# Performance work log

Measured on AMD Instinct MI355X. Metric: run time of the kernel, lower is better.

## Reference

```python
import jax, jax.numpy as jnp
import numpy as np

IN_DIM = 128
OUT_DIM = 128
ATTN_DIM = 64
N_REL = 200
N_NODE = 50000
N_EDGE = 500000
N_QUERY = 64
COE_TIMEDIFF = 0.2  # computed in torch code but unused downstream


def setup_inputs() -> dict:
    key = jax.random.key(0)
    ks = jax.random.split(key, 24)
    # edges: [E,7] with columns (r_idx, _, rel, _, tau, sub, obj)
    r_idx = jax.random.randint(ks[0], (N_EDGE,), 0, N_QUERY)
    rel = jax.random.randint(ks[1], (N_EDGE,), 0, 2 * N_REL + 1)
    tau = jax.random.randint(ks[2], (N_EDGE,), -1, 366)  # -1 triggers the where() fallback
    sub = jax.random.randint(ks[3], (N_EDGE,), 0, N_NODE)
    obj = jax.random.randint(ks[4], (N_EDGE,), 0, N_NODE)
    fill = jnp.zeros((N_EDGE,), jnp.int64 if jax.config.jax_enable_x64 else jnp.int32)
    edges = jnp.stack([r_idx, fill, rel, fill, tau, sub, obj], axis=1)
    s = 1.0 / np.sqrt(IN_DIM)
    sa = 1.0 / np.sqrt(ATTN_DIM)
    return {
        "q_sub": jax.random.randint(ks[5], (N_QUERY,), 0, N_NODE),
        "q_rel": jax.random.randint(ks[6], (N_QUERY,), 0, 2 * N_REL + 1),
        "q_tau": jax.random.randint(ks[7], (N_QUERY,), 0, 366),
        "hidden": jax.random.normal(ks[8], (N_NODE, IN_DIM), jnp.float32),
        "edges": edges,
        "n_node": N_NODE,
        "old_nodes_new_idx": jax.random.randint(ks[9], (10000,), 0, N_NODE),
        "rela_embed": jax.random.normal(ks[10], (2 * N_REL + 1, IN_DIM), jnp.float32),
        "Ws": jax.random.normal(ks[11], (IN_DIM, ATTN_DIM), jnp.float32) * s,
        "Wr": jax.random.normal(ks[12], (IN_DIM, ATTN_DIM), jnp.float32) * s,
        "Wqr_W": jax.random.normal(ks[13], (IN_DIM, ATTN_DIM), jnp.float32) * s,
        "Wqr_b": jax.random.normal(ks[14], (ATTN_DIM,), jnp.float32) * s,
        "Wtau": jax.random.normal(ks[15], (IN_DIM, ATTN_DIM), jnp.float32) * s,
        "w_alpha_W": jax.random.normal(ks[16], (ATTN_DIM, 1), jnp.float32) * sa,
        "w_alpha_b": jax.random.normal(ks[17], (1,), jnp.float32) * sa,
        "Wh": jax.random.normal(ks[18], (IN_DIM, OUT_DIM), jnp.float32) * s,
        "wt1": jax.random.normal(ks[19], (1, IN_DIM), jnp.float32),
        "bt1": jax.random.normal(ks[20], (1, IN_DIM), jnp.float32),
        "wt2": jax.random.normal(ks[21], (1, IN_DIM), jnp.float32),
        "bt2": jax.random.normal(ks[22], (1, IN_DIM), jnp.float32),
    }


def reference(q_sub, q_rel, q_tau, hidden, edges, n_node, old_nodes_new_idx,
              rela_embed, Ws, Wr, Wqr_W, Wqr_b, Wtau, w_alpha_W, w_alpha_b,
              Wh, wt1, bt1, wt2, bt2):
    r_idx = edges[:, 0]
    rel = edges[:, 2]
    tau = edges[:, 4]
    sub = edges[:, 5]
    obj = edges[:, 6]
    hs = hidden[sub]                      # [E, in_dim] gather
    hr = rela_embed[rel]                  # [E, in_dim]
    h_qr = rela_embed[q_rel][r_idx]       # [E, in_dim]
    taus_q = q_tau[r_idx]
    tau = jnp.where(tau >= 0, tau, taus_q)
    delta_tau = (tau - taus_q).astype(hidden.dtype)[:, None]  # [E,1]
    h_tau = wt1 * delta_tau + bt1 + jnp.sin(wt2 * delta_tau + bt2)  # [E, in_dim]
    message = hs + hr + h_tau
    pre = jax.nn.relu(hs @ Ws + hr @ Wr + (h_qr @ Wqr_W + Wqr_b) + h_tau @ Wtau)
    alpha = jax.nn.sigmoid(pre @ w_alpha_W + w_alpha_b)  # [E,1]
    msg_agg = jax.ops.segment_sum(alpha * message, obj, num_segments=n_node)
    return msg_agg @ Wh  # act is identity by default
```

## Files before the change

kernel.cpp:

```cpp
#include <hip/hip_runtime.h>
#include <hip/hip_fp16.h>

#define IN_DIM   128
#define OUT_DIM  128
#define ATTN_DIM 64
#define N_RELV   401
#define N_NODE   50000
#define N_EDGE   500000
#define N_QUERY  64
#define N_DT     731
#define CAP      40

#define NBW_NODE 782
#define NBW_REL  7
#define NBW_DT   12
#define NBW_QR   1
#define NBW_ZERO 13
#define RB0      NBW_NODE
#define DB0      (NBW_NODE + NBW_REL)
#define QB0      (DB0 + NBW_DT)
#define ZB0      (QB0 + NBW_QR)
#define FB0      (ZB0 + NBW_ZERO)
#define NB_TOT   (FB0 + 1)

typedef unsigned short ushort_t;
typedef unsigned int   uint_t;
typedef __attribute__((ext_vector_type(8))) short v8s;
typedef __attribute__((ext_vector_type(4))) float v4f;

__device__ __forceinline__ int clampi(int v, int lo, int hi) {
    return v < lo ? lo : (v > hi ? hi : v);
}
__device__ __forceinline__ float bu2f(ushort_t u) {
    union { uint_t i; float f; } v; v.i = ((uint_t)u) << 16; return v.f;
}
__device__ __forceinline__ float blo(uint_t u) { return bu2f((ushort_t)(u & 0xffff)); }
__device__ __forceinline__ float bhi(uint_t u) { return bu2f((ushort_t)(u >> 16)); }
__device__ __forceinline__ ushort_t f2bu(float f) {
    union { float f; uint_t i; } v; v.f = f;
    const uint_t x = v.i;
    return (ushort_t)((x + 0x7fffu + ((x >> 16) & 1u)) >> 16);
}
__device__ __forceinline__ uint_t cvtpk(float a, float b) {
    uint_t r;
    asm("v_cvt_pk_bf16_f32 %0, %1, %2" : "=v"(r) : "v"(a), "v"(b));
    return r;
}

__device__ __forceinline__ int swz_byte(int row, int byte_in_row) {
    return (row * 256 + byte_in_row) ^ ((row & 7) << 4);
}

__device__ __forceinline__ void stage_w64(ushort_t* shw, const float* __restrict__ W,
                                          int tid) {
    #pragma unroll
    for (int i = 0; i < 4; ++i) {
        const int pi = tid + 256 * i;
        const int kp = pi >> 4;
        const int n4 = (pi & 15) * 4;
        const float4 A = *(const float4*)(W + (size_t)(2 * kp) * 64 + n4);
        const float4 B = *(const float4*)(W + (size_t)(2 * kp + 1) * 64 + n4);
        const float Aa[4] = {A.x, A.y, A.z, A.w};
        const float Ba[4] = {B.x, B.y, B.z, B.w};
        #pragma unroll
        for (int j = 0; j < 4; ++j)
            *(uint_t*)((char*)shw + swz_byte(n4 + j, kp * 4)) = cvtpk(Aa[j], Ba[j]);
    }
}
__device__ __forceinline__ void stage_w128(ushort_t* shw, const float* __restrict__ W,
                                           int tid) {
    #pragma unroll
    for (int i = 0; i < 8; ++i) {
        const int pi = tid + 256 * i;
        const int kp = pi >> 5;
        const int n4 = (pi & 31) * 4;
        const float4 A = *(const float4*)(W + (size_t)(2 * kp) * 128 + n4);
        const float4 B = *(const float4*)(W + (size_t)(2 * kp + 1) * 128 + n4);
        const float Aa[4] = {A.x, A.y, A.z, A.w};
        const float Ba[4] = {B.x, B.y, B.z, B.w};
        #pragma unroll
        for (int j = 0; j < 4; ++j)
            *(uint_t*)((char*)shw + swz_byte(64 + n4 + j, kp * 4)) = cvtpk(Aa[j], Ba[j]);
    }
}
__device__ __forceinline__ void load_x_rows(const float* __restrict__ X, int rowc,
                                            int q, v8s hfr[4]) {
    #pragma unroll
    for (int c = 0; c < 4; ++c) {
        const float4 f0 = *(const float4*)(X + (size_t)rowc * 128 + 32 * c + 8 * q);
        const float4 f1 = *(const float4*)(X + (size_t)rowc * 128 + 32 * c + 8 * q + 4);
        union { v8s s; uint4 u; } uu;
        uu.u = make_uint4(cvtpk(f0.x, f0.y), cvtpk(f0.z, f0.w),
                          cvtpk(f1.x, f1.y), cvtpk(f1.z, f1.w));
        hfr[c] = uu.s;
    }
}
__device__ __forceinline__ void mfma_store(const ushort_t* shw, const v8s hfr[4],
                                           int row, int Nlim,
                                           ushort_t* __restrict__ attn_out,
                                           ushort_t* __restrict__ msg_out,
                                           int m16, int q) {
    #pragma unroll
    for (int t = 0; t < 12; ++t) {
        v4f acc = {0.f, 0.f, 0.f, 0.f};
        #pragma unroll
        for (int c = 0; c < 4; ++c) {
            const v8s wfr = *(const v8s*)((const char*)shw +
                              swz_byte(16 * t + m16, (32 * c + 8 * q) * 2));
            acc = __builtin_amdgcn_mfma_f32_16x16x32_bf16(wfr, hfr[c], acc, 0, 0, 0);
        }
        if (row < Nlim) {
            const uint_t u0 = cvtpk(acc[0], acc[1]);
            const uint_t u1 = cvtpk(acc[2], acc[3]);
            const int dim = 16 * t + 4 * q;
            if (dim < 64)
                *(uint2*)(attn_out + (size_t)row * 64 + dim) = make_uint2(u0, u1);
            else
                *(uint2*)(msg_out + (size_t)row * 128 + (dim - 64)) = make_uint2(u0, u1);
        }
    }
}

__global__ __launch_bounds__(256) void fused_pre(
    const float* __restrict__ hidden, const float* __restrict__ Ws,
    const float* __restrict__ Wh,   const float* __restrict__ rela,
    const float* __restrict__ Wr,   const float* __restrict__ Wtau,
    const float* __restrict__ wt1,  const float* __restrict__ bt1,
    const float* __restrict__ wt2,  const float* __restrict__ bt2,
    const int* __restrict__ q_rel,  const float* __restrict__ WqrW,
    const float* __restrict__ Wqrb, const int* __restrict__ edges,
    ushort_t* __restrict__ node_attn, ushort_t* __restrict__ node_msg,
    ushort_t* __restrict__ rel_attn,  ushort_t* __restrict__ rel_msg,
    ushort_t* __restrict__ dt_attn,   ushort_t* __restrict__ dt_msg,
    ushort_t* __restrict__ Xqr,
    int* __restrict__ flag, int* __restrict__ cnt, int* __restrict__ ovfn)
{
    __shared__ ushort_t shw[192 * 128];
    const int bid = blockIdx.x, tid = threadIdx.x;
    const int wid = tid >> 6, lane = tid & 63;
    const int m16 = lane & 15, q = lane >> 4;

    if (bid < NBW_NODE) {
        stage_w64 (shw, Ws, tid);
        stage_w128(shw, Wh, tid);
        __syncthreads();
        const int row  = bid * 64 + wid * 16 + m16;
        const int rowc = row < N_NODE ? row : N_NODE - 1;
        v8s hfr[4];
        load_x_rows(hidden, rowc, q, hfr);
        mfma_store(shw, hfr, row, N_NODE, node_attn, node_msg, m16, q);
    } else if (bid < DB0) {
        stage_w64 (shw, Wr, tid);
        stage_w128(shw, Wh, tid);
        __syncthreads();
        const int row  = (bid - RB0) * 64 + wid * 16 + m16;
        const int rowc = row < N_RELV ? row : N_RELV - 1;
        v8s hfr[4];
        load_x_rows(rela, rowc, q, hfr);
        mfma_store(shw, hfr, row, N_RELV, rel_attn, rel_msg, m16, q);
    } else if (bid < QB0) {
        stage_w64 (shw, Wtau, tid);
        stage_w128(shw, Wh, tid);
        __syncthreads();
        const int row  = (bid - DB0) * 64 + wid * 16 + m16;
        const int rowc = row < N_DT ? row : N_DT - 1;
        const float dtv = (float)(rowc - 365);
        v8s hfr[4];
        #pragma unroll
        for (int c = 0; c < 4; ++c) {
            const int o = 32 * c + 8 * q;
            const float4 w1a = *(const float4*)(wt1 + o), w1b = *(const float4*)(wt1 + o + 4);
            const float4 b1a = *(const float4*)(bt1 + o), b1b = *(const float4*)(bt1 + o + 4);
            const float4 w2a = *(const float4*)(wt2 + o), w2b = *(const float4*)(wt2 + o + 4);
            const float4 b2a = *(const float4*)(bt2 + o), b2b = *(const float4*)(bt2 + o + 4);
            const float h0 = w1a.x * dtv + b1a.x + sinf(w2a.x * dtv + b2a.x);
            const float h1 = w1a.y * dtv + b1a.y + sinf(w2a.y * dtv + b2a.y);
            const float h2 = w1a.z * dtv + b1a.z + sinf(w2a.z * dtv + b2a.z);
            const float h3 = w1a.w * dtv + b1a.w + sinf(w2a.w * dtv + b2a.w);
            const float h4 = w1b.x * dtv + b1b.x + sinf(w2b.x * dtv + b2b.x);
            const float h5 = w1b.y * dtv + b1b.y + sinf(w2b.y * dtv + b2b.y);
            const float h6 = w1b.z * dtv + b1b.z + sinf(w2b.z * dtv + b2b.z);
            const float h7 = w1b.w * dtv + b1b.w + sinf(w2b.w * dtv + b2b.w);
            union { v8s s; uint4 u; } uu;
            uu.u = make_uint4(cvtpk(h0, h1), cvtpk(h2, h3), cvtpk(h4, h5), cvtpk(h6, h7));
            hfr[c] = uu.s;
        }
        mfma_store(shw, hfr, row, N_DT, dt_attn, dt_msg, m16, q);
    } else if (bid < ZB0) {
        int* ok = (int*)shw;
        if (tid == 0) *ok = 1;
        __syncthreads();
        int badv = 0;
        for (int t = tid; t < 1000; t += 256) {
            const int w = edges[2 * t + 1];
            if (w != 0 && w != -1) badv = 1;
        }
        if (badv) *ok = 0;
        __syncthreads();
        const int i64 = *ok;
        __syncthreads();

        stage_w64(shw, WqrW, tid);
        __syncthreads();
        const int qrow = wid * 16 + m16;
        const int relq = clampi(q_rel[i64 ? 2 * qrow : qrow], 0, N_RELV - 1);
        v8s hfr[4];
        load_x_rows(rela, relq, q, hfr);
        #pragma unroll
        for (int t = 0; t < 4; ++t) {
            v4f acc = {0.f, 0.f, 0.f, 0.f};
            #pragma unroll
            for (int c = 0; c < 4; ++c) {
                const v8s wfr = *(const v8s*)((const char*)shw +
                                  swz_byte(16 * t + m16, (32 * c + 8 * q) * 2));
                acc = __builtin_amdgcn_mfma_f32_16x16x32_bf16(wfr, hfr[c], acc, 0, 0, 0);
            }
            const int dim = 16 * t + 4 * q;
            const float4 bi = *(const float4*)(Wqrb + dim);
            const uint_t u0 = cvtpk(acc[0] + bi.x, acc[1] + bi.y);
            const uint_t u1 = cvtpk(acc[2] + bi.z, acc[3] + bi.w);
            *(uint2*)(Xqr + (size_t)qrow * 64 + dim) = make_uint2(u0, u1);
        }
    } else if (bid < FB0) {
        int4* c4 = (int4*)cnt;
        const int b = (bid - ZB0) * 256 + tid;
        #pragma unroll
        for (int k = 0; k < 4; ++k) {
            const int i4 = b * 4 + k;
            if (i4 < N_NODE / 4) c4[i4] = make_int4(0, 0, 0, 0);
        }
    } else {
        int* ok = (int*)shw;
        if (tid == 0) *ok = 0;
        __syncthreads();
        int badv = 0;
        for (int t = tid; t < 1000; t += 256) {
            const int w = edges[2 * t + 1];
            if (w != 0 && w != -1) badv = 1;
        }
        if (badv) *ok = 1;
        __syncthreads();
        if (tid == 0) { flag[0] = (*ok == 0) ? 1 : 0; ovfn[0] = 0; }
    }
}

__device__ __forceinline__ float dot8(uint4 xs, uint4 xr, uint4 xt, uint4 xq,
                                      float4 wA, float4 wB)
{
    float s0, s1, v;
    s0 = blo(xs.x) + blo(xr.x) + blo(xt.x) + blo(xq.x);
    s1 = bhi(xs.x) + bhi(xr.x) + bhi(xt.x) + bhi(xq.x);
    v  = fmaxf(s0, 0.f) * wA.x + fmaxf(s1, 0.f) * wA.y;
    s0 = blo(xs.y) + blo(xr.y) + blo(xt.y) + blo(xq.y);
    s1 = bhi(xs.y) + bhi(xr.y) + bhi(xt.y) + bhi(xq.y);
    v += fmaxf(s0, 0.f) * wA.z + fmaxf(s1, 0.f) * wA.w;
    s0 = blo(xs.z) + blo(xr.z) + blo(xt.z) + blo(xq.z);
    s1 = bhi(xs.z) + bhi(xr.z) + bhi(xt.z) + bhi(xq.z);
    v += fmaxf(s0, 0.f) * wB.x + fmaxf(s1, 0.f) * wB.y;
    s0 = blo(xs.w) + blo(xr.w) + blo(xt.w) + blo(xq.w);
    s1 = bhi(xs.w) + bhi(xr.w) + bhi(xt.w) + bhi(xq.w);
    v += fmaxf(s0, 0.f) * wB.z + fmaxf(s1, 0.f) * wB.w;
    return v;
}

__global__ __launch_bounds__(256) void alpha_scatter(
    const int* __restrict__ edges, const int* __restrict__ q_tau,
    const ushort_t* __restrict__ node_attn, const ushort_t* __restrict__ rel_attn,
    const ushort_t* __restrict__ dt_attn,  const ushort_t* __restrict__ Xqr,
    const float* __restrict__ w_alpha_W, const float* __restrict__ w_alpha_b,
    const int* __restrict__ flag, int* __restrict__ cnt,
    int2* __restrict__ meta, int* __restrict__ ovfn, int4* __restrict__ ovfl)
{
    const int g   = threadIdx.x & 7;
    const int grp = threadIdx.x >> 3;
    const int e0r = blockIdx.x * 128 + grp * 4;
    const int e0  = e0r <= N_EDGE - 4 ? e0r : N_EDGE - 4;
    const int i64 = flag[0];

    const float4 wA = *(const float4*)(w_alpha_W + 8 * g);
    const float4 wB = *(const float4*)(w_alpha_W + 8 * g + 4);

    int r0, rel0, tau0, sub0, obj0, r1, rel1, tau1, sub1, obj1;
    int r2, rel2, tau2, sub2, obj2, r3, rel3, tau3, sub3, obj3;
    if (!i64) {
        const int4 ev = *(const int4*)(edges + (size_t)e0 * 7 + 4 * (g < 6 ? g : 6));
        #define GETF(j) __shfl(((j) & 3) == 0 ? ev.x : ((j) & 3) == 1 ? ev.y : \
                               ((j) & 3) == 2 ? ev.z : ev.w, (j) >> 2, 8)
        r0 = GETF(0);  rel0 = GETF(2);  tau0 = GETF(4);  sub0 = GETF(5);  obj0 = GETF(6);
        r1 = GETF(7);  rel1 = GETF(9);  tau1 = GETF(11); sub1 = GETF(12); obj1 = GETF(13);
        r2 = GETF(14); rel2 = GETF(16); tau2 = GETF(18); sub2 = GETF(19); obj2 = GETF(20);
        r3 = GETF(21); rel3 = GETF(23); tau3 = GETF(25); sub3 = GETF(26); obj3 = GETF(27);
        #undef GETF
    } else {
        const int* E0 = edges + (size_t)(e0    ) * 14;
        const int* E1 = edges + (size_t)(e0 + 1) * 14;
        const int* E2 = edges + (size_t)(e0 + 2) * 14;
        const int* E3 = edges + (size_t)(e0 + 3) * 14;
        r0 = E0[0]; rel0 = E0[4]; tau0 = E0[8]; sub0 = E0[10]; obj0 = E0[12];
        r1 = E1[0]; rel1 = E1[4]; tau1 = E1[8]; sub1 = E1[10]; obj1 = E1[12];
        r2 = E2[0]; rel2 = E2[4]; tau2 = E2[8]; sub2 = E2[10]; obj2 = E2[12];
        r3 = E3[0]; rel3 = E3[4]; tau3 = E3[8]; sub3 = E3[10]; obj3 = E3[12];
    }
    r0 = clampi(r0, 0, N_QUERY - 1); rel0 = clampi(rel0, 0, N_RELV - 1);
    sub0 = clampi(sub0, 0, N_NODE - 1); obj0 = clampi(obj0, 0, N_NODE - 1);
    r1 = clampi(r1, 0, N_QUERY - 1); rel1 = clampi(rel1, 0, N_RELV - 1);
    sub1 = clampi(sub1, 0, N_NODE - 1); obj1 = clampi(obj1, 0, N_NODE - 1);
    r2 = clampi(r2, 0, N_QUERY - 1); rel2 = clampi(rel2, 0, N_RELV - 1);
    sub2 = clampi(sub2, 0, N_NODE - 1); obj2 = clampi(obj2, 0, N_NODE - 1);
    r3 = clampi(r3, 0, N_QUERY - 1); rel3 = clampi(rel3, 0, N_RELV - 1);
    sub3 = clampi(sub3, 0, N_NODE - 1); obj3 = clampi(obj3, 0, N_NODE - 1);

    const int tq0 = q_tau[i64 ? 2 * r0 : r0];
    const int tq1 = q_tau[i64 ? 2 * r1 : r1];
    const int tq2 = q_tau[i64 ? 2 * r2 : r2];
    const int tq3 = q_tau[i64 ? 2 * r3 : r3];
    if (tau0 < 0) tau0 = tq0;
    if (tau1 < 0) tau1 = tq1;
    if (tau2 < 0) tau2 = tq2;
    if (tau3 < 0) tau3 = tq3;
    const int di0 = clampi(tau0 - tq0 + 365, 0, N_DT - 1);
    const int di1 = clampi(tau1 - tq1 + 365, 0, N_DT - 1);
    const int di2 = clampi(tau2 - tq2 + 365, 0, N_DT - 1);
    const int di3 = clampi(tau3 - tq3 + 365, 0, N_DT - 1);

    const uint4 xs0 = *(const uint4*)(node_attn + (size_t)sub0 * ATTN_DIM + 8 * g);
    const uint4 xr0 = *(const uint4*)(rel_attn + (size_t)rel0 * ATTN_DIM + 8 * g);
    const uint4 xt0 = *(const uint4*)(dt_attn  + (size_t)di0  * ATTN_DIM + 8 * g);
    const uint4 xq0 = *(const uint4*)(Xqr      + (size_t)r0   * ATTN_DIM + 8 * g);
    const uint4 xs1 = *(const uint4*)(node_attn + (size_t)sub1 * ATTN_DIM + 8 * g);
    const uint4 xr1 = *(const uint4*)(rel_attn + (size_t)rel1 * ATTN_DIM + 8 * g);
    const uint4 xt1 = *(const uint4*)(dt_attn  + (size_t)di1  * ATTN_DIM + 8 * g);
    const uint4 xq1 = *(const uint4*)(Xqr      + (size_t)r1   * ATTN_DIM + 8 * g);
    const uint4 xs2 = *(const uint4*)(node_attn + (size_t)sub2 * ATTN_DIM + 8 * g);
    const uint4 xr2 = *(const uint4*)(rel_attn + (size_t)rel2 * ATTN_DIM + 8 * g);
    const uint4 xt2 = *(const uint4*)(dt_attn  + (size_t)di2  * ATTN_DIM + 8 * g);
    const uint4 xq2 = *(const uint4*)(Xqr      + (size_t)r2   * ATTN_DIM + 8 * g);
    const uint4 xs3 = *(const uint4*)(node_attn + (size_t)sub3 * ATTN_DIM + 8 * g);
    const uint4 xr3 = *(const uint4*)(rel_attn + (size_t)rel3 * ATTN_DIM + 8 * g);
    const uint4 xt3 = *(const uint4*)(dt_attn  + (size_t)di3  * ATTN_DIM + 8 * g);
    const uint4 xq3 = *(const uint4*)(Xqr      + (size_t)r3   * ATTN_DIM + 8 * g);

    float v0 = dot8(xs0, xr0, xt0, xq0, wA, wB);
    float v1 = dot8(xs1, xr1, xt1, xq1, wA, wB);
    float v2 = dot8(xs2, xr2, xt2, xq2, wA, wB);
    float v3 = dot8(xs3, xr3, xt3, xq3, wA, wB);

    #pragma unroll
    for (int off = 4; off > 0; off >>= 1) {
        v0 += __shfl_xor(v0, off, 8);
        v1 += __shfl_xor(v1, off, 8);
        v2 += __shfl_xor(v2, off, 8);
        v3 += __shfl_xor(v3, off, 8);
    }

    if (g < 4 && e0r + g < N_EDGE) {
        const float vg  = g == 0 ? v0 : (g == 1 ? v1 : (g == 2 ? v2 : v3));
        const int objg  = g == 0 ? obj0 : (g == 1 ? obj1 : (g == 2 ? obj2 : obj3));
        const int subg  = g == 0 ? sub0 : (g == 1 ? sub1 : (g == 2 ? sub2 : sub3));
        const int dig   = g == 0 ? di0  : (g == 1 ? di1  : (g == 2 ? di2  : di3));
        const int relg  = g == 0 ? rel0 : (g == 1 ? rel1 : (g == 2 ? rel2 : rel3));
        const float alpha = 1.f / (1.f + __expf(-(vg + w_alpha_b[0])));
        const int pos = atomicAdd(&cnt[objg], 1);
        if (pos < CAP) {
            const uint_t px = (uint_t)subg | ((uint_t)dig << 17) | ((uint_t)(relg & 31) << 27);
            const uint_t py = (uint_t)(relg >> 5) |
                              ((uint_t)__half_as_ushort(__float2half_rn(alpha)) << 16);
            meta[(size_t)pos * N_NODE + objg] = make_int2((int)px, (int)py);
        } else {
            const int ov = atomicAdd(ovfn, 1);
            if (ov < N_EDGE)
                ovfl[ov] = make_int4(subg | (dig << 17), relg | (objg << 9),
                                     __float_as_int(alpha), 0);
        }
    }
}

__device__ __forceinline__ void agg_edge(
    int2 m, int l32,
    const ushort_t* __restrict__ node_msg, const ushort_t* __restrict__ rel_msg,
    const ushort_t* __restrict__ dt_msg,
    float& a0, float& a1, float& a2, float& a3)
{
    const int sub = m.x & 0x1FFFF;
    const int di  = ((uint_t)m.x >> 17) & 0x3FF;
    const int rel = (((uint_t)m.x >> 27) & 31) | (((uint_t)m.y & 0xF) << 5);
    const float al = __half2float(__ushort_as_half((ushort_t)((uint_t)m.y >> 16)));
    const uint2 am = *(const uint2*)(node_msg + (size_t)sub * 128 + 4 * l32);
    const uint2 bm = *(const uint2*)(rel_msg  + (size_t)rel * 128 + 4 * l32);
    const uint2 tm = *(const uint2*)(dt_msg   + (size_t)di  * 128 + 4 * l32);
    a0 += al * (blo(am.x) + blo(bm.x) + blo(tm.x));
    a1 += al * (bhi(am.x) + bhi(bm.x) + bhi(tm.x));
    a2 += al * (blo(am.y) + blo(bm.y) + blo(tm.y));
    a3 += al * (bhi(am.y) + bhi(bm.y) + bhi(tm.y));
}

__global__ __launch_bounds__(256) void agg_kernel(
    const int* __restrict__ cnt, const int2* __restrict__ meta,
    const int* __restrict__ ovfn, const int4* __restrict__ ovfl,
    const ushort_t* __restrict__ node_msg, const ushort_t* __restrict__ rel_msg,
    const ushort_t* __restrict__ dt_msg, float* __restrict__ out)
{
    const int lane = threadIdx.x & 63;
    const int half = lane >> 5;
    const int l32  = lane & 31;
    const int n    = blockIdx.x * 4 + (threadIdx.x >> 6);

    int m = cnt[n]; if (m > CAP) m = CAP;
    float a0 = 0.f, a1 = 0.f, a2 = 0.f, a3 = 0.f;

    int j = 0;
    for (; j + 7 < m; j += 8) {
        const int2 ma = meta[(size_t)(j     + half) * N_NODE + n];
        const int2 mb = meta[(size_t)(j + 2 + half) * N_NODE + n];
        const int2 mc = meta[(size_t)(j + 4 + half) * N_NODE + n];
        const int2 md = meta[(size_t)(j + 6 + half) * N_NODE + n];
        agg_edge(ma, l32, node_msg, rel_msg, dt_msg, a0, a1, a2, a3);
        agg_edge(mb, l32, node_msg, rel_msg, dt_msg, a0, a1, a2, a3);
        agg_edge(mc, l32, node_msg, rel_msg, dt_msg, a0, a1, a2, a3);
        agg_edge(md, l32, node_msg, rel_msg, dt_msg, a0, a1, a2, a3);
    }
    for (; j + 1 < m; j += 2) {
        const int2 ma = meta[(size_t)(j + half) * N_NODE + n];
        agg_edge(ma, l32, node_msg, rel_msg, dt_msg, a0, a1, a2, a3);
    }
    if (j < m && half == 0) {
        const int2 ma = meta[(size_t)j * N_NODE + n];
        agg_edge(ma, l32, node_msg, rel_msg, dt_msg, a0, a1, a2, a3);
    }

    int nov = ovfn[0]; if (nov > N_EDGE) nov = N_EDGE;
    for (int i = 0; i < nov; ++i) {
        const int4 mo = ovfl[i];
        const int objo = (int)((uint_t)mo.y >> 9);
        if (objo != n || half != 0) continue;
        const int subo = mo.x & 0x1FFFF;
        const int dio  = (int)((uint_t)mo.x >> 17);
        const int relo = mo.y & 0x1FF;
        const float alo = __int_as_float(mo.z);
        const uint2 am = *(const uint2*)(node_msg + (size_t)subo * 128 + 4 * l32);
        const uint2 bm = *(const uint2*)(rel_msg  + (size_t)relo * 128 + 4 * l32);
        const uint2 tm = *(const uint2*)(dt_msg   + (size_t)dio  * 128 + 4 * l32);
        a0 += alo * (blo(am.x) + blo(bm.x) + blo(tm.x));
        a1 += alo * (bhi(am.x) + bhi(bm.x) + bhi(tm.x));
        a2 += alo * (blo(am.y) + blo(bm.y) + blo(tm.y));
        a3 += alo * (bhi(am.y) + bhi(bm.y) + bhi(tm.y));
    }

    a0 += __shfl_xor(a0, 32, 64);
    a1 += __shfl_xor(a1, 32, 64);
    a2 += __shfl_xor(a2, 32, 64);
    a3 += __shfl_xor(a3, 32, 64);

    if (half == 0) {
        float4 o; o.x = a0; o.y = a1; o.z = a2; o.w = a3;
        *(float4*)(out + (size_t)n * OUT_DIM + 4 * l32) = o;
    }
}

__device__ __forceinline__ void parse_edge(const int* __restrict__ edges, int e,
                                           int i64, int& r, int& rel, int& tau,
                                           int& sub, int& obj) {
    if (i64) {
        const int* E = edges + (size_t)e * 14;
        r = E[0]; rel = E[4]; tau = E[8]; sub = E[10]; obj = E[12];
    } else {
        const int* E = edges + (size_t)e * 7;
        r = E[0]; rel = E[2]; tau = E[4]; sub = E[5]; obj = E[6];
    }
    r   = clampi(r,   0, N_QUERY - 1);
    rel = clampi(rel, 0, N_RELV - 1);
    sub = clampi(sub, 0, N_NODE - 1);
    obj = clampi(obj, 0, N_NODE - 1);
}

__global__ __launch_bounds__(256) void edge_atomic_kernel(
    const int* __restrict__ edges, const int* __restrict__ q_tau,
    const ushort_t* __restrict__ node_attn, const ushort_t* __restrict__ node_msg,
    const ushort_t* __restrict__ rel_attn,  const ushort_t* __restrict__ rel_msg,
    const ushort_t* __restrict__ dt_attn,   const ushort_t* __restrict__ dt_msg,
    const ushort_t* __restrict__ Xqr,
    const float* __restrict__ w_alpha_W, const float* __restrict__ w_alpha_b,
    const int* __restrict__ flag, float* __restrict__ out)
{
    const int lane = threadIdx.x & 63;
    const int e    = blockIdx.x * 4 + (threadIdx.x >> 6);
    const int i64  = flag[0];

    int r, rel, tau, sub, obj;
    parse_edge(edges, e, i64, r, rel, tau, sub, obj);
    const int tq = q_tau[i64 ? 2 * r : r];
    if (tau < 0) tau = tq;
    const int di = clampi(tau - tq + 365, 0, N_DT - 1);

    const float xs = bu2f(node_attn[(size_t)sub * ATTN_DIM + lane]);
    const float xr = bu2f(rel_attn[(size_t)rel * ATTN_DIM + lane]);
    const float xt = bu2f(dt_attn[(size_t)di  * ATTN_DIM + lane]);
    const float xq = bu2f(Xqr[(size_t)r * ATTN_DIM + lane]);

    float v = fmaxf(xs + xr + xq + xt, 0.f) * w_alpha_W[lane];
    #pragma unroll
    for (int off = 32; off > 0; off >>= 1)
        v += __shfl_down(v, off, 64);
    v = __shfl(v, 0, 64);
    const float alpha = 1.f / (1.f + __expf(-(v + w_alpha_b[0])));

    const uint_t am = *(const uint_t*)(node_msg + (size_t)sub * 128 + 2 * lane);
    const uint_t bm = *(const uint_t*)(rel_msg  + (size_t)rel * 128 + 2 * lane);
    const uint_t tm = *(const uint_t*)(dt_msg   + (size_t)di  * 128 + 2 * lane);
    const float mx = blo(am) + blo(bm) + blo(tm);
    const float my = bhi(am) + bhi(bm) + bhi(tm);

    float* dst = out + (size_t)obj * OUT_DIM;
    atomicAdd(dst + 2 * lane,     alpha * mx);
    atomicAdd(dst + 2 * lane + 1, alpha * my);
}

extern "C" void kernel_launch(void* const* d_in, const int* in_sizes, int n_in,
                              void* d_out, int out_size, void* d_ws, size_t ws_size,
                              hipStream_t stream)
{
    const int*   q_rel  = (const int*)d_in[1];
    const int*   q_tau  = (const int*)d_in[2];
    const float* hidden = (const float*)d_in[3];
    const int*   edges  = (const int*)d_in[4];
    const float* rela   = (const float*)d_in[7];
    const float* Ws     = (const float*)d_in[8];
    const float* Wr     = (const float*)d_in[9];
    const float* WqrW   = (const float*)d_in[10];
    const float* Wqrb   = (const float*)d_in[11];
    const float* Wtau   = (const float*)d_in[12];
    const float* waW    = (const float*)d_in[13];
    const float* wab    = (const float*)d_in[14];
    const float* Wh     = (const float*)d_in[15];
    const float* wt1    = (const float*)d_in[16];
    const float* bt1    = (const float*)d_in[17];
    const float* wt2    = (const float*)d_in[18];
    const float* bt2    = (const float*)d_in[19];
    float* out = (float*)d_out;

    char* p = (char*)d_ws;
    size_t off = 0;
    auto carve = [&](size_t bytes) {
        char* q = p + off;
        off = (off + bytes + 255) & ~(size_t)255;
        return q;
    };
    int*      flag      = (int*)     carve(64);
    int*      cnt       = (int*)     carve((size_t)N_NODE * 4);
    int*      ovfn      = (int*)     carve(64);
    ushort_t* XqrB      = (ushort_t*)carve((size_t)N_QUERY * ATTN_DIM * 2);
    ushort_t* rel_attn  = (ushort_t*)carve((size_t)N_RELV * ATTN_DIM * 2);
    ushort_t* rel_msg   = (ushort_t*)carve((size_t)N_RELV * OUT_DIM * 2);
    ushort_t* dt_attn   = (ushort_t*)carve((size_t)N_DT * ATTN_DIM * 2);
    ushort_t* dt_msg    = (ushort_t*)carve((size_t)N_DT * OUT_DIM * 2);
    ushort_t* node_attn = (ushort_t*)carve((size_t)N_NODE * ATTN_DIM * 2);
    ushort_t* node_msg  = (ushort_t*)carve((size_t)N_NODE * OUT_DIM * 2);
    int2*     meta      = (int2*)    carve((size_t)N_NODE * CAP * 8);
    int4*     ovfl      = (int4*)    carve((size_t)N_EDGE * 16);
    const size_t need_full = off;

    fused_pre<<<NB_TOT, 256, 0, stream>>>(
        hidden, Ws, Wh, rela, Wr, Wtau, wt1, bt1, wt2, bt2,
        q_rel, WqrW, Wqrb, edges,
        node_attn, node_msg, rel_attn, rel_msg, dt_attn, dt_msg, XqrB,
        flag, cnt, ovfn);

    if (ws_size >= need_full) {
        alpha_scatter<<<(N_EDGE + 127) / 128, 256, 0, stream>>>(
            edges, q_tau, node_attn, rel_attn, dt_attn, XqrB,
            waW, wab, flag, cnt, meta, ovfn, ovfl);
        agg_kernel<<<N_NODE / 4, 256, 0, stream>>>(cnt, meta, ovfn, ovfl,
                                                   node_msg, rel_msg, dt_msg, out);
    } else {
        (void)hipMemsetAsync(out, 0, (size_t)out_size * sizeof(float), stream);
        edge_atomic_kernel<<<N_EDGE / 4, 256, 0, stream>>>(edges, q_tau,
                                                           node_attn, node_msg,
                                                           rel_attn, rel_msg,
                                                           dt_attn, dt_msg, XqrB,
                                                           waW, wab, flag, out);
    }
}
```

Baseline: 197.8 us.

## Enlarge fused_pre blocks to 512 threads with two row tiles per wave

The precompute kernel now runs 512-thread blocks in which each wave processes two 16-row tiles, so one block covers 256 rows instead of 64. Each shared-memory weight fragment is reused for two MFMAs, and there are about four times fewer blocks, each staging the bf16 weights. This cuts redundant weight staging and LDS reads, at the cost of more registers per thread and fewer blocks to spread across CUs. The zeroing and flag-check branches are adjusted for the larger block.

New measurement: 207.4 us. 4.9% more time.

```diff
diff --git a/kernel.cpp b/kernel.cpp
--- a/kernel.cpp
+++ b/kernel.cpp
@@ -11,11 +11,11 @@
 #define N_DT     731
 #define CAP      40
 
-#define NBW_NODE 782
-#define NBW_REL  7
-#define NBW_DT   12
+#define NBW_NODE 196
+#define NBW_REL  2
+#define NBW_DT   3
 #define NBW_QR   1
-#define NBW_ZERO 13
+#define NBW_ZERO 7
 #define RB0      NBW_NODE
 #define DB0      (NBW_NODE + NBW_REL)
 #define QB0      (DB0 + NBW_DT)
@@ -36,11 +36,6 @@
 }
 __device__ __forceinline__ float blo(uint_t u) { return bu2f((ushort_t)(u & 0xffff)); }
 __device__ __forceinline__ float bhi(uint_t u) { return bu2f((ushort_t)(u >> 16)); }
-__device__ __forceinline__ ushort_t f2bu(float f) {
-    union { float f; uint_t i; } v; v.f = f;
-    const uint_t x = v.i;
-    return (ushort_t)((x + 0x7fffu + ((x >> 16) & 1u)) >> 16);
-}
 __device__ __forceinline__ uint_t cvtpk(float a, float b) {
     uint_t r;
     asm("v_cvt_pk_bf16_f32 %0, %1, %2" : "=v"(r) : "v"(a), "v"(b));
@@ -54,8 +49,8 @@
 __device__ __forceinline__ void stage_w64(ushort_t* shw, const float* __restrict__ W,
                                           int tid) {
     #pragma unroll
-    for (int i = 0; i < 4; ++i) {
-        const int pi = tid + 256 * i;
+    for (int i = 0; i < 2; ++i) {
+        const int pi = tid + 512 * i;
         const int kp = pi >> 4;
         const int n4 = (pi & 15) * 4;
         const float4 A = *(const float4*)(W + (size_t)(2 * kp) * 64 + n4);
@@ -70,8 +65,8 @@
 __device__ __forceinline__ void stage_w128(ushort_t* shw, const float* __restrict__ W,
                                            int tid) {
     #pragma unroll
-    for (int i = 0; i < 8; ++i) {
-        const int pi = tid + 256 * i;
+    for (int i = 0; i < 4; ++i) {
+        const int pi = tid + 512 * i;
         const int kp = pi >> 5;
         const int n4 = (pi & 31) * 4;
         const float4 A = *(const float4*)(W + (size_t)(2 * kp) * 128 + n4);
@@ -95,33 +90,44 @@
         hfr[c] = uu.s;
     }
 }
-__device__ __forceinline__ void mfma_store(const ushort_t* shw, const v8s hfr[4],
-                                           int row, int Nlim,
-                                           ushort_t* __restrict__ attn_out,
-                                           ushort_t* __restrict__ msg_out,
-                                           int m16, int q) {
+__device__ __forceinline__ void mfma_store2(const ushort_t* shw,
+                                            const v8s h0[4], const v8s h1[4],
+                                            int row0, int row1, int Nlim,
+                                            ushort_t* __restrict__ attn_out,
+                                            ushort_t* __restrict__ msg_out,
+                                            int m16, int q) {
     #pragma unroll
     for (int t = 0; t < 12; ++t) {
-        v4f acc = {0.f, 0.f, 0.f, 0.f};
+        v4f a0 = {0.f, 0.f, 0.f, 0.f};
+        v4f a1 = {0.f, 0.f, 0.f, 0.f};
         #pragma unroll
         for (int c = 0; c < 4; ++c) {
             const v8s wfr = *(const v8s*)((const char*)shw +
                               swz_byte(16 * t + m16, (32 * c + 8 * q) * 2));
-            acc = __builtin_amdgcn_mfma_f32_16x16x32_bf16(wfr, hfr[c], acc, 0, 0, 0);
-        }
-        if (row < Nlim) {
-            const uint_t u0 = cvtpk(acc[0], acc[1]);
-            const uint_t u1 = cvtpk(acc[2], acc[3]);
-            const int dim = 16 * t + 4 * q;
+            a0 = __builtin_amdgcn_mfma_f32_16x16x32_bf16(wfr, h0[c], a0, 0, 0, 0);
+            a1 = __builtin_amdgcn_mfma_f32_16x16x32_bf16(wfr, h1[c], a1, 0, 0, 0);
+        }
+        const int dim = 16 * t + 4 * q;
+        if (row0 < Nlim) {
+            const uint_t u0 = cvtpk(a0[0], a0[1]);
+            const uint_t u1 = cvtpk(a0[2], a0[3]);
             if (dim < 64)
-                *(uint2*)(attn_out + (size_t)row * 64 + dim) = make_uint2(u0, u1);
+                *(uint2*)(attn_out + (size_t)row0 * 64 + dim) = make_uint2(u0, u1);
             else
-                *(uint2*)(msg_out + (size_t)row * 128 + (dim - 64)) = make_uint2(u0, u1);
-        }
-    }
-}
-
-__global__ __launch_bounds__(256) void fused_pre(
+                *(uint2*)(msg_out + (size_t)row0 * 128 + (dim - 64)) = make_uint2(u0, u1);
+        }
+        if (row1 < Nlim) {
+            const uint_t u0 = cvtpk(a1[0], a1[1]);
+            const uint_t u1 = cvtpk(a1[2], a1[3]);
+            if (dim < 64)
+                *(uint2*)(attn_out + (size_t)row1 * 64 + dim) = make_uint2(u0, u1);
+            else
+                *(uint2*)(msg_out + (size_t)row1 * 128 + (dim - 64)) = make_uint2(u0, u1);
+        }
+    }
+}
+
+__global__ __launch_bounds__(512) void fused_pre(
     const float* __restrict__ hidden, const float* __restrict__ Ws,
     const float* __restrict__ Wh,   const float* __restrict__ rela,
     const float* __restrict__ Wr,   const float* __restrict__ Wtau,
@@ -144,28 +150,37 @@
         stage_w64 (shw, Ws, tid);
         stage_w128(shw, Wh, tid);
         __syncthreads();
-        const int row  = bid * 64 + wid * 16 + m16;
-        const int rowc = row < N_NODE ? row : N_NODE - 1;
-        v8s hfr[4];
-        load_x_rows(hidden, rowc, q, hfr);
-        mfma_store(shw, hfr, row, N_NODE, node_attn, node_msg, m16, q);
+        const int base = bid * 256 + wid * 32;
+        const int row0 = base + m16, row1 = base + 16 + m16;
+        const int rc0  = row0 < N_NODE ? row0 : N_NODE - 1;
+        const int rc1  = row1 < N_NODE ? row1 : N_NODE - 1;
+        v8s h0[4], h1[4];
+        load_x_rows(hidden, rc0, q, h0);
+        load_x_rows(hidden, rc1, q, h1);
+        mfma_store2(shw, h0, h1, row0, row1, N_NODE, node_attn, node_msg, m16, q);
     } else if (bid < DB0) {
         stage_w64 (shw, Wr, tid);
         stage_w128(shw, Wh, tid);
         __syncthreads();
-        const int row  = (bid - RB0) * 64 + wid * 16 + m16;
-        const int rowc = row < N_RELV ? row : N_RELV - 1;
-        v8s hfr[4];
-        load_x_rows(rela, rowc, q, hfr);
-        mfma_store(shw, hfr, row, N_RELV, rel_attn, rel_msg, m16, q);
+        const int base = (bid - RB0) * 256 + wid * 32;
+        const int row0 = base + m16, row1 = base + 16 + m16;
+        const int rc0  = row0 < N_RELV ? row0 : N_RELV - 1;
+        const int rc1  = row1 < N_RELV ? row1 : N_RELV - 1;
+        v8s h0[4], h1[4];
+        load_x_rows(rela, rc0, q, h0);
+        load_x_rows(rela, rc1, q, h1);
+        mfma_store2(shw, h0, h1, row0, row1, N_RELV, rel_attn, rel_msg, m16, q);
     } else if (bid < QB0) {
         stage_w64 (shw, Wtau, tid);
         stage_w128(shw, Wh, tid);
         __syncthreads();
-        const int row  = (bid - DB0) * 64 + wid * 16 + m16;
-        const int rowc = row < N_DT ? row : N_DT - 1;
-        const float dtv = (float)(rowc - 365);
-        v8s hfr[4];
+        const int base = (bid - DB0) * 256 + wid * 32;
+        const int row0 = base + m16, row1 = base + 16 + m16;
+        const int rc0  = row0 < N_DT ? row0 : N_DT - 1;
+        const int rc1  = row1 < N_DT ? row1 : N_DT - 1;
+        const float dtv0 = (float)(rc0 - 365);
+        const float dtv1 = (float)(rc1 - 365);
+        v8s h0[4], h1[4];
         #pragma unroll
         for (int c = 0; c < 4; ++c) {
             const int o = 32 * c + 8 * q;
@@ -173,25 +188,30 @@
             const float4 b1a = *(const float4*)(bt1 + o), b1b = *(const float4*)(bt1 + o + 4);
             const float4 w2a = *(const float4*)(wt2 + o), w2b = *(const float4*)(wt2 + o + 4);
             const float4 b2a = *(const float4*)(bt2 + o), b2b = *(const float4*)(bt2 + o + 4);
-            const float h0 = w1a.x * dtv + b1a.x + sinf(w2a.x * dtv + b2a.x);
-            const float h1 = w1a.y * dtv + b1a.y + sinf(w2a.y * dtv + b2a.y);
-            const float h2 = w1a.z * dtv + b1a.z + sinf(w2a.z * dtv + b2a.z);
-            const float h3 = w1a.w * dtv + b1a.w + sinf(w2a.w * dtv + b2a.w);
-            const float h4 = w1b.x * dtv + b1b.x + sinf(w2b.x * dtv + b2b.x);
-            const float h5 = w1b.y * dtv + b1b.y + sinf(w2b.y * dtv + b2b.y);
-            const float h6 = w1b.z * dtv + b1b.z + sinf(w2b.z * dtv + b2b.z);
-            const float h7 = w1b.w * dtv + b1b.w + sinf(w2b.w * dtv + b2b.w);
-            union { v8s s; uint4 u; } uu;
-            uu.u = make_uint4(cvtpk(h0, h1), cvtpk(h2, h3), cvtpk(h4, h5), cvtpk(h6, h7));
-            hfr[c] = uu.s;
-        }
-        mfma_store(shw, hfr, row, N_DT, dt_attn, dt_msg, m16, q);
+            const float w1v[8] = {w1a.x, w1a.y, w1a.z, w1a.w, w1b.x, w1b.y, w1b.z, w1b.w};
+            const float b1v[8] = {b1a.x, b1a.y, b1a.z, b1a.w, b1b.x, b1b.y, b1b.z, b1b.w};
+            const float w2v[8] = {w2a.x, w2a.y, w2a.z, w2a.w, w2b.x, w2b.y, w2b.z, w2b.w};
+            const float b2v[8] = {b2a.x, b2a.y, b2a.z, b2a.w, b2b.x, b2b.y, b2b.z, b2b.w};
+            float e0[8], e1[8];
+            #pragma unroll
+            for (int j = 0; j < 8; ++j) {
+                e0[j] = w1v[j] * dtv0 + b1v[j] + sinf(w2v[j] * dtv0 + b2v[j]);
+                e1[j] = w1v[j] * dtv1 + b1v[j] + sinf(w2v[j] * dtv1 + b2v[j]);
+            }
+            union { v8s s; uint4 u; } u0, u1;
+            u0.u = make_uint4(cvtpk(e0[0], e0[1]), cvtpk(e0[2], e0[3]),
+                              cvtpk(e0[4], e0[5]), cvtpk(e0[6], e0[7]));
+            u1.u = make_uint4(cvtpk(e1[0], e1[1]), cvtpk(e1[2], e1[3]),
+                              cvtpk(e1[4], e1[5]), cvtpk(e1[6], e1[7]));
+            h0[c] = u0.s; h1[c] = u1.s;
+        }
+        mfma_store2(shw, h0, h1, row0, row1, N_DT, dt_attn, dt_msg, m16, q);
     } else if (bid < ZB0) {
         int* ok = (int*)shw;
         if (tid == 0) *ok = 1;
         __syncthreads();
         int badv = 0;
-        for (int t = tid; t < 1000; t += 256) {
+        for (int t = tid; t < 1000; t += 512) {
             const int w = edges[2 * t + 1];
             if (w != 0 && w != -1) badv = 1;
         }
@@ -202,31 +222,33 @@
 
         stage_w64(shw, WqrW, tid);
         __syncthreads();
-        const int qrow = wid * 16 + m16;
-        const int relq = clampi(q_rel[i64 ? 2 * qrow : qrow], 0, N_RELV - 1);
-        v8s hfr[4];
-        load_x_rows(rela, relq, q, hfr);
-        #pragma unroll
-        for (int t = 0; t < 4; ++t) {
-            v4f acc = {0.f, 0.f, 0.f, 0.f};
+        if (wid < 4) {
+            const int qrow = wid * 16 + m16;
+            const int relq = clampi(q_rel[i64 ? 2 * qrow : qrow], 0, N_RELV - 1);
+            v8s hfr[4];
+            load_x_rows(rela, relq, q, hfr);
             #pragma unroll
-            for (int c = 0; c < 4; ++c) {
-                const v8s wfr = *(const v8s*)((const char*)shw +
-                                  swz_byte(16 * t + m16, (32 * c + 8 * q) * 2));
-                acc = __builtin_amdgcn_mfma_f32_16x16x32_bf16(wfr, hfr[c], acc, 0, 0, 0);
+            for (int t = 0; t < 4; ++t) {
+                v4f acc = {0.f, 0.f, 0.f, 0.f};
+                #pragma unroll
+                for (int c = 0; c < 4; ++c) {
+                    const v8s wfr = *(const v8s*)((const char*)shw +
+                                      swz_byte(16 * t + m16, (32 * c + 8 * q) * 2));
+                    acc = __builtin_amdgcn_mfma_f32_16x16x32_bf16(wfr, hfr[c], acc, 0, 0, 0);
+                }
+                const int dim = 16 * t + 4 * q;
+                const float4 bi = *(const float4*)(Wqrb + dim);
+                const uint_t u0 = cvtpk(acc[0] + bi.x, acc[1] + bi.y);
+                const uint_t u1 = cvtpk(acc[2] + bi.z, acc[3] + bi.w);
+                *(uint2*)(Xqr + (size_t)qrow * 64 + dim) = make_uint2(u0, u1);
             }
-            const int dim = 16 * t + 4 * q;
-            const float4 bi = *(const float4*)(Wqrb + dim);
-            const uint_t u0 = cvtpk(acc[0] + bi.x, acc[1] + bi.y);
-            const uint_t u1 = cvtpk(acc[2] + bi.z, acc[3] + bi.w);
-            *(uint2*)(Xqr + (size_t)qrow * 64 + dim) = make_uint2(u0, u1);
         }
     } else if (bid < FB0) {
         int4* c4 = (int4*)cnt;
-        const int b = (bid - ZB0) * 256 + tid;
+        const int b = (bid - ZB0) * 512 + tid;
         #pragma unroll
         for (int k = 0; k < 4; ++k) {
-            const int i4 = b * 4 + k;
+            const int i4 = b + k * 3584;
             if (i4 < N_NODE / 4) c4[i4] = make_int4(0, 0, 0, 0);
         }
     } else {
@@ -234,7 +256,7 @@
         if (tid == 0) *ok = 0;
         __syncthreads();
         int badv = 0;
-        for (int t = tid; t < 1000; t += 256) {
+        for (int t = tid; t < 1000; t += 512) {
             const int w = edges[2 * t + 1];
             if (w != 0 && w != -1) badv = 1;
         }
@@ -559,7 +581,7 @@
     int4*     ovfl      = (int4*)    carve((size_t)N_EDGE * 16);
     const size_t need_full = off;
 
-    fused_pre<<<NB_TOT, 256, 0, stream>>>(
+    fused_pre<<<NB_TOT, 512, 0, stream>>>(
         hidden, Ws, Wh, rela, Wr, Wtau, wt1, bt1, wt2, bt2,
         q_rel, WqrW, Wqrb, edges,
         node_attn, node_msg, rel_attn, rel_msg, dt_attn, dt_msg, XqrB,
```
